# Kernel tuning notes

Measured on AMD Instinct MI355X. Metric: run time of the kernel, lower is better.

## Reference

```python
import jax, jax.numpy as jnp
import numpy as np

N, IN_DIM, MLPW, HID, NCLS = 2048, 1024, 16, 256, 4


def setup_inputs() -> dict:
    key = jax.random.key(0)
    ks = jax.random.split(key, 12)
    f32 = jnp.float32
    return {
        "x": jax.random.normal(ks[0], (N, IN_DIM), f32),
        "adj": jax.random.uniform(ks[1], (N, N), f32),
        "xdeg": jax.random.uniform(ks[2], (N, N), f32),
        "ydeg": jax.random.uniform(ks[3], (N, N), f32),
        # edge MLP([3, mlp_width, 2])
        "Wm1": jax.random.normal(ks[4], (3, MLPW), f32) * (1.0 / np.sqrt(3.0)),
        "bm1": jnp.zeros((MLPW,), f32),
        "Wm2": jax.random.normal(ks[5], (MLPW, 2), f32) * (1.0 / np.sqrt(MLPW)),
        "bm2": jnp.zeros((2,), f32),
        # GCN / dense layers (stored as [in, out]; torch Linear applies x @ W.T)
        "Wg1": jax.random.normal(ks[6], (IN_DIM, HID), f32) * (1.0 / np.sqrt(IN_DIM)),
        "Wl2": jax.random.normal(ks[7], (HID, 64), f32) * (1.0 / np.sqrt(HID)),
        "bl2": jnp.zeros((64,), f32),
        "Wg2": jax.random.normal(ks[8], (64, NCLS), f32) * (1.0 / 8.0),
    }


def reference(x, adj, xdeg, ydeg, Wm1, bm1, Wm2, bm2, Wg1, Wl2, bl2, Wg2):
    n = adj.shape[0]
    # Edge-feature MLP mask. The torch code gathers nonzero entries, runs the
    # MLP, scatters back into a zero buffer, then multiplies by adj. Computing
    # the mask densely is mathematically identical because adj * mask is zero
    # wherever adj is zero.
    feats = jnp.stack([adj, xdeg, ydeg], axis=-1)          # [N, N, 3]
    h = jax.nn.relu(feats @ Wm1 + bm1)                     # [N, N, MLPW]
    mask = jax.nn.softmax(h @ Wm2 + bm2, axis=-1)[..., 1]  # [N, N]
    A = adj * mask + jnp.eye(n, dtype=adj.dtype)
    # Symmetric-ish normalization: D_row^{-1/2} A D_col^{-1/2}
    # (the torch diag-matmul chain reduces to this row/col scaling).
    rowsum = jnp.sum(A, axis=1)
    colsum = jnp.sum(A, axis=0)
    dr = jnp.where(rowsum > 0, jax.lax.rsqrt(jnp.where(rowsum > 0, rowsum, 1.0)), 0.0)
    dc = jnp.where(colsum > 0, jax.lax.rsqrt(jnp.where(colsum > 0, colsum, 1.0)), 0.0)
    A = dr[:, None] * A * dc[None, :]
    # GCN layer 1 (dropout = identity in eval mode)
    hid = (A @ (x @ Wg1)) @ Wl2 + bl2                      # [N, 64]
    # GCN layer 2
    out = A @ (hid @ Wg2)                                  # [N, n_classes]
    return out, hid
```

## Files before the change

kernel.cpp:

```cpp
#include <hip/hip_runtime.h>

#define NN 2048
#define MLPW 16

typedef __attribute__((ext_vector_type(8))) short short8v;
typedef __attribute__((ext_vector_type(16))) float float16v;
typedef __attribute__((ext_vector_type(4))) unsigned short ushort4v;
typedef __attribute__((ext_vector_type(8))) unsigned short ushort8v;

__device__ __forceinline__ unsigned short f2b(float f) {
  unsigned int u = __float_as_uint(f);
  unsigned int r = (u + 0x7fffu + ((u >> 16) & 1u)) >> 16;
  return (unsigned short)r;
}
__device__ __forceinline__ float b2f(unsigned short u) {
  return __uint_as_float(((unsigned int)u) << 16);
}

__global__ void __launch_bounds__(256) prep_wT_kernel(
    const float* __restrict__ Wg1, unsigned short* __restrict__ wT) {
  const int n = blockIdx.x, tid = threadIdx.x;
  for (int k = tid; k < 1024; k += 256)
    wT[(size_t)n * 1024 + k] = f2b(Wg1[(size_t)k * 256 + n]);
}

__global__ void __launch_bounds__(256) edge_kernel(
    const float* __restrict__ adj, const float* __restrict__ xdeg,
    const float* __restrict__ ydeg,
    const float* __restrict__ Wm1, const float* __restrict__ bm1,
    const float* __restrict__ Wm2, const float* __restrict__ bm2,
    unsigned short* __restrict__ Abf, float* __restrict__ dr) {
  __shared__ float w1[48], b1[16], w2[32], b2s[2];
  __shared__ float wsum[4];
  const int tid = threadIdx.x;
  if (tid < 48) w1[tid] = Wm1[tid];
  if (tid < 16) b1[tid] = bm1[tid];
  if (tid < 32) w2[tid] = Wm2[tid];
  if (tid < 2) b2s[tid] = bm2[tid];
  __syncthreads();
  const int i = blockIdx.x;
  const float4* adj4 = (const float4*)(adj + (size_t)i * NN);
  const float4* xd4 = (const float4*)(xdeg + (size_t)i * NN);
  const float4* yd4 = (const float4*)(ydeg + (size_t)i * NN);
  ushort4v* A4 = (ushort4v*)(Abf + (size_t)i * NN);
  float rsum = 0.f;
  for (int j4 = tid; j4 < NN / 4; j4 += 256) {
    float4 av = adj4[j4], xv = xd4[j4], yv = yd4[j4];
    float aa[4] = {av.x, av.y, av.z, av.w};
    float xx[4] = {xv.x, xv.y, xv.z, xv.w};
    float yy[4] = {yv.x, yv.y, yv.z, yv.w};
    ushort4v oo;
#pragma unroll
    for (int e = 0; e < 4; e++) {
      float l0 = b2s[0], l1 = b2s[1];
#pragma unroll
      for (int k = 0; k < MLPW; k++) {
        float h = fmaf(aa[e], w1[k], fmaf(xx[e], w1[16 + k], fmaf(yy[e], w1[32 + k], b1[k])));
        h = fmaxf(h, 0.f);
        l0 = fmaf(h, w2[2 * k], l0);
        l1 = fmaf(h, w2[2 * k + 1], l1);
      }
      float mask = 1.f / (1.f + __expf(l0 - l1));
      float v = aa[e] * mask;
      int j = j4 * 4 + e;
      if (j == i) v += 1.f;
      oo[e] = f2b(v);
      rsum += v;
    }
    A4[j4] = oo;
  }
#pragma unroll
  for (int off = 32; off > 0; off >>= 1) rsum += __shfl_down(rsum, off);
  if ((tid & 63) == 0) wsum[tid >> 6] = rsum;
  __syncthreads();
  if (tid == 0) {
    float t = wsum[0] + wsum[1] + wsum[2] + wsum[3];
    dr[i] = t > 0.f ? rsqrtf(t) : 0.f;
  }
}

__global__ void __launch_bounds__(256) colsum_partial_kernel(
    const unsigned short* __restrict__ Abf, float* __restrict__ partial) {
  const int j = blockIdx.x * 256 + threadIdx.x;
  const int i0 = blockIdx.y * (NN / 32);
  float s = 0.f;
  for (int i = i0; i < i0 + NN / 32; i++) s += b2f(Abf[(size_t)i * NN + j]);
  partial[(size_t)blockIdx.y * NN + j] = s;
}

__global__ void __launch_bounds__(256) dc_kernel(
    const float* __restrict__ partial, float* __restrict__ dc) {
  const int j = blockIdx.x * 256 + threadIdx.x;
  float s = 0.f;
#pragma unroll
  for (int p = 0; p < 32; p++) s += partial[(size_t)p * NN + j];
  dc[j] = s > 0.f ? rsqrtf(s) : 0.f;
}

template <bool B_F32>
__global__ void __launch_bounds__(256) gemm_splitk_kernel(
    const unsigned short* __restrict__ A, const void* __restrict__ Bv,
    float* __restrict__ P, int M, int N, int K, int Kc) {
  __shared__ unsigned short As[32 * 80];
  __shared__ unsigned short Bs[128 * 80];
  const int tid = threadIdx.x;
  const int lane = tid & 63, wave = tid >> 6;
  const int l31 = lane & 31, half = lane >> 5;
  const int row0 = blockIdx.y * 32, col0 = blockIdx.x * 128;
  const int kbeg = blockIdx.z * Kc;

  float16v acc;
#pragma unroll
  for (int r = 0; r < 16; r++) acc[r] = 0.f;

  for (int k0 = 0; k0 < Kc; k0 += 64) {
    {
      const int r = tid >> 3, c = tid & 7;
      *(ushort8v*)&As[r * 80 + c * 8] =
          *(const ushort8v*)&A[(size_t)(row0 + r) * K + kbeg + k0 + c * 8];
    }
#pragma unroll
    for (int i = 0; i < 4; i++) {
      const int id = tid + i * 256;
      const int r = id >> 3, c = id & 7;
      if (B_F32) {
        const float* bp = (const float*)Bv + (size_t)(col0 + r) * K + kbeg + k0 + c * 8;
        float4 u = *(const float4*)bp, v = *(const float4*)(bp + 4);
        ushort8v pk = {f2b(u.x), f2b(u.y), f2b(u.z), f2b(u.w),
                       f2b(v.x), f2b(v.y), f2b(v.z), f2b(v.w)};
        *(ushort8v*)&Bs[r * 80 + c * 8] = pk;
      } else {
        *(ushort8v*)&Bs[r * 80 + c * 8] =
            *(const ushort8v*)&((const unsigned short*)Bv)[(size_t)(col0 + r) * K + kbeg + k0 + c * 8];
      }
    }
    __syncthreads();
#pragma unroll
    for (int ks = 0; ks < 4; ks++) {
      short8v a = *(const short8v*)&As[l31 * 80 + ks * 16 + half * 8];
      short8v b = *(const short8v*)&Bs[(wave * 32 + l31) * 80 + ks * 16 + half * 8];
      acc = __builtin_amdgcn_mfma_f32_32x32x16_bf16(a, b, acc, 0, 0, 0);
    }
    __syncthreads();
  }
  float* Pb = P + ((size_t)blockIdx.z * M + row0) * N + col0 + wave * 32 + l31;
#pragma unroll
  for (int reg = 0; reg < 16; reg++) {
    const int m = (reg & 3) + 8 * (reg >> 2) + 4 * half;
    Pb[(size_t)m * N] = acc[reg];
  }
}

__global__ void __launch_bounds__(256) reduce_xwt_kernel(
    const float* __restrict__ P, const float* __restrict__ dc,
    unsigned short* __restrict__ XWT) {
  const int t = blockIdx.x * 256 + threadIdx.x;
  const int i = t >> 8;
  const int j0 = (t & 255) * 8;
  float s[8] = {0, 0, 0, 0, 0, 0, 0, 0};
#pragma unroll
  for (int sk = 0; sk < 4; sk++) {
    const float* p = P + ((size_t)sk * 256 + i) * 2048 + j0;
    float4 u = *(const float4*)p, v = *(const float4*)(p + 4);
    s[0] += u.x; s[1] += u.y; s[2] += u.z; s[3] += u.w;
    s[4] += v.x; s[5] += v.y; s[6] += v.z; s[7] += v.w;
  }
  float4 d0 = *(const float4*)&dc[j0], d1 = *(const float4*)&dc[j0 + 4];
  ushort8v o = {f2b(s[0] * d0.x), f2b(s[1] * d0.y), f2b(s[2] * d0.z), f2b(s[3] * d0.w),
                f2b(s[4] * d1.x), f2b(s[5] * d1.y), f2b(s[6] * d1.z), f2b(s[7] * d1.w)};
  *(ushort8v*)&XWT[(size_t)i * 2048 + j0] = o;
}

__global__ void __launch_bounds__(256) tail_kernel(
    const float* __restrict__ P2, const float* __restrict__ dr,
    const float* __restrict__ dc, const float* __restrict__ Wl2,
    const float* __restrict__ bl2, const float* __restrict__ Wg2,
    float* __restrict__ hid, float* __restrict__ HW) {
  __shared__ float T1s[16][256];
  __shared__ float hidS[16][68];
  const int m0 = blockIdx.x * 16;
  const int tid = threadIdx.x;
#pragma unroll
  for (int i = 0; i < 16; i++) {
    const int idx = tid + i * 256;
    const int mi = idx >> 8, n = idx & 255;
    float s = 0.f;
#pragma unroll
    for (int sk = 0; sk < 4; sk++)
      s += P2[((size_t)sk * 2048 + m0 + mi) * 256 + n];
    T1s[mi][n] = s * dr[m0 + mi];
  }
  __syncthreads();
  const int j = tid & 63, mg = tid >> 6;
  float h[4] = {bl2[j], bl2[j], bl2[j], bl2[j]};
  for (int n = 0; n < 256; n++) {
    float w = Wl2[(size_t)n * 64 + j];
#pragma unroll
    for (int r = 0; r < 4; r++) h[r] = fmaf(T1s[mg * 4 + r][n], w, h[r]);
  }
#pragma unroll
  for (int r = 0; r < 4; r++) {
    hid[(size_t)(m0 + mg * 4 + r) * 64 + j] = h[r];
    hidS[mg * 4 + r][j] = h[r];
  }
  __syncthreads();
  if (tid < 64) {
    const int r = tid >> 2, c = tid & 3;
    float s = 0.f;
#pragma unroll
    for (int jj = 0; jj < 64; jj++) s = fmaf(hidS[r][jj], Wg2[jj * 4 + c], s);
    HW[(size_t)(m0 + r) * 4 + c] = s * dc[m0 + r];
  }
}

__global__ void __launch_bounds__(256) out_kernel(
    const unsigned short* __restrict__ Abf, const float* __restrict__ HW,
    const float* __restrict__ dr, float* __restrict__ outp) {
  const int i = blockIdx.x, tid = threadIdx.x;
  const ushort8v a8 = ((const ushort8v*)(Abf + (size_t)i * NN))[tid];
  const float4* hw4 = (const float4*)HW;
  const int j0 = tid * 8;
  float ax = 0.f, ay = 0.f, az = 0.f, aw = 0.f;
#pragma unroll
  for (int e = 0; e < 8; e++) {
    float a = b2f(a8[e]);
    float4 h = hw4[j0 + e];
    ax = fmaf(a, h.x, ax);
    ay = fmaf(a, h.y, ay);
    az = fmaf(a, h.z, az);
    aw = fmaf(a, h.w, aw);
  }
  __shared__ float red[4][256];
  red[0][tid] = ax; red[1][tid] = ay; red[2][tid] = az; red[3][tid] = aw;
  __syncthreads();
  for (int s = 128; s > 0; s >>= 1) {
    if (tid < s) {
      red[0][tid] += red[0][tid + s];
      red[1][tid] += red[1][tid + s];
      red[2][tid] += red[2][tid + s];
      red[3][tid] += red[3][tid + s];
    }
    __syncthreads();
  }
  if (tid < 4) outp[(size_t)i * 4 + tid] = dr[i] * red[tid][0];
}

extern "C" void kernel_launch(void* const* d_in, const int* in_sizes, int n_in,
                              void* d_out, int out_size, void* d_ws, size_t ws_size,
                              hipStream_t stream) {
  const float* x    = (const float*)d_in[0];
  const float* adj  = (const float*)d_in[1];
  const float* xdeg = (const float*)d_in[2];
  const float* ydeg = (const float*)d_in[3];
  const float* Wm1  = (const float*)d_in[4];
  const float* bm1  = (const float*)d_in[5];
  const float* Wm2  = (const float*)d_in[6];
  const float* bm2  = (const float*)d_in[7];
  const float* Wg1  = (const float*)d_in[8];
  const float* Wl2  = (const float*)d_in[9];
  const float* bl2  = (const float*)d_in[10];
  const float* Wg2  = (const float*)d_in[11];

  char* ws = (char*)d_ws;
  unsigned short* Abf  = (unsigned short*)(ws);
  unsigned short* Wg1T = (unsigned short*)(ws + 8388608);
  unsigned short* XWT  = (unsigned short*)(ws + 8912896);
  float* P    = (float*)(ws + 9961472);
  float* part = (float*)(ws + 18350080);
  float* dr   = (float*)(ws + 18612224);
  float* dc   = (float*)(ws + 18620416);
  float* HW   = (float*)(ws + 18628608);

  float* outp = (float*)d_out;
  float* hid  = (float*)d_out + 2048 * 4;

  prep_wT_kernel<<<256, 256, 0, stream>>>(Wg1, Wg1T);
  edge_kernel<<<NN, 256, 0, stream>>>(adj, xdeg, ydeg, Wm1, bm1, Wm2, bm2, Abf, dr);
  colsum_partial_kernel<<<dim3(NN / 256, 32), 256, 0, stream>>>(Abf, part);
  dc_kernel<<<NN / 256, 256, 0, stream>>>(part, dc);
  gemm_splitk_kernel<true><<<dim3(2048 / 128, 256 / 32, 4), 256, 0, stream>>>(
      Wg1T, x, P, 256, 2048, 1024, 256);
  reduce_xwt_kernel<<<256, 256, 0, stream>>>(P, dc, XWT);
  gemm_splitk_kernel<false><<<dim3(256 / 128, 2048 / 32, 4), 256, 0, stream>>>(
      Abf, XWT, P, 2048, 256, 2048, 512);
  tail_kernel<<<2048 / 16, 256, 0, stream>>>(P, dr, dc, Wl2, bl2, Wg2, hid, HW);
  out_kernel<<<NN, 256, 0, stream>>>(Abf, HW, dr, outp);
}
```

Before: 179.0 us.

## Tile Wg1 transpose, vectorize colsum, deepen GEMM K-tile and raise split-K

The Wg1 transpose now goes through a shared-memory tile so both reads and writes are coalesced, and the column-sum kernel reads eight bf16 values per thread with 32 row blocks. The split-K GEMM stages a 128-wide K slab per iteration, which halves the number of barriers, and the A@XW GEMM uses split-K 8 instead of 4 to launch more blocks. In exchange the GEMM uses more shared memory, which can lower occupancy, and the tail kernel has to reduce twice as many fp32 partials. The workspace layout is rearranged to hold the larger partial buffer.

```diff
diff --git a/kernel.cpp b/kernel.cpp
--- a/kernel.cpp
+++ b/kernel.cpp
@@ -19,9 +19,30 @@
 
 __global__ void __launch_bounds__(256) prep_wT_kernel(
     const float* __restrict__ Wg1, unsigned short* __restrict__ wT) {
-  const int n = blockIdx.x, tid = threadIdx.x;
-  for (int k = tid; k < 1024; k += 256)
-    wT[(size_t)n * 1024 + k] = f2b(Wg1[(size_t)k * 256 + n]);
+  __shared__ float T[64][65];
+  const int k0 = blockIdx.x * 64, n0 = blockIdx.y * 64;
+  const int tid = threadIdx.x;
+  const int kr = tid >> 2, ch = tid & 3;
+  const float* src = Wg1 + (size_t)(k0 + kr) * 256 + n0 + ch * 16;
+#pragma unroll
+  for (int q = 0; q < 4; q++) {
+    float4 v = ((const float4*)src)[q];
+    T[kr][ch * 16 + q * 4 + 0] = v.x;
+    T[kr][ch * 16 + q * 4 + 1] = v.y;
+    T[kr][ch * 16 + q * 4 + 2] = v.z;
+    T[kr][ch * 16 + q * 4 + 3] = v.w;
+  }
+  __syncthreads();
+  const int nr = kr, kc = ch;
+  ushort8v o0, o1;
+#pragma unroll
+  for (int e = 0; e < 8; e++) {
+    o0[e] = f2b(T[kc * 16 + e][nr]);
+    o1[e] = f2b(T[kc * 16 + 8 + e][nr]);
+  }
+  unsigned short* dst = wT + (size_t)(n0 + nr) * 1024 + k0 + kc * 16;
+  *(ushort8v*)dst = o0;
+  *(ushort8v*)(dst + 8) = o1;
 }
 
 __global__ void __launch_bounds__(256) edge_kernel(
@@ -79,13 +100,19 @@
   }
 }
 
-__global__ void __launch_bounds__(256) colsum_partial_kernel(
+__global__ void __launch_bounds__(256) colsum_kernel(
     const unsigned short* __restrict__ Abf, float* __restrict__ partial) {
-  const int j = blockIdx.x * 256 + threadIdx.x;
-  const int i0 = blockIdx.y * (NN / 32);
-  float s = 0.f;
-  for (int i = i0; i < i0 + NN / 32; i++) s += b2f(Abf[(size_t)i * NN + j]);
-  partial[(size_t)blockIdx.y * NN + j] = s;
+  const int j0 = threadIdx.x * 8;
+  const int i0 = blockIdx.x * 64;
+  float s[8] = {0, 0, 0, 0, 0, 0, 0, 0};
+  for (int i = 0; i < 64; i++) {
+    ushort8v a = *(const ushort8v*)&Abf[(size_t)(i0 + i) * NN + j0];
+#pragma unroll
+    for (int e = 0; e < 8; e++) s[e] += b2f(a[e]);
+  }
+  float* p = partial + (size_t)blockIdx.x * NN + j0;
+  *(float4*)p = make_float4(s[0], s[1], s[2], s[3]);
+  *(float4*)(p + 4) = make_float4(s[4], s[5], s[6], s[7]);
 }
 
 __global__ void __launch_bounds__(256) dc_kernel(
@@ -101,8 +128,9 @@
 __global__ void __launch_bounds__(256) gemm_splitk_kernel(
     const unsigned short* __restrict__ A, const void* __restrict__ Bv,
     float* __restrict__ P, int M, int N, int K, int Kc) {
-  __shared__ unsigned short As[32 * 80];
-  __shared__ unsigned short Bs[128 * 80];
+  constexpr int SW = 136;
+  __shared__ unsigned short As[32 * SW];
+  __shared__ unsigned short Bs[128 * SW];
   const int tid = threadIdx.x;
   const int lane = tid & 63, wave = tid >> 6;
   const int l31 = lane & 31, half = lane >> 5;
@@ -113,32 +141,34 @@
 #pragma unroll
   for (int r = 0; r < 16; r++) acc[r] = 0.f;
 
-  for (int k0 = 0; k0 < Kc; k0 += 64) {
-    {
-      const int r = tid >> 3, c = tid & 7;
-      *(ushort8v*)&As[r * 80 + c * 8] =
+  for (int k0 = 0; k0 < Kc; k0 += 128) {
+#pragma unroll
+    for (int i = 0; i < 2; i++) {
+      const int id = tid + i * 256;
+      const int r = id >> 4, c = id & 15;
+      *(ushort8v*)&As[r * SW + c * 8] =
           *(const ushort8v*)&A[(size_t)(row0 + r) * K + kbeg + k0 + c * 8];
     }
 #pragma unroll
-    for (int i = 0; i < 4; i++) {
+    for (int i = 0; i < 8; i++) {
       const int id = tid + i * 256;
-      const int r = id >> 3, c = id & 7;
+      const int r = id >> 4, c = id & 15;
       if (B_F32) {
         const float* bp = (const float*)Bv + (size_t)(col0 + r) * K + kbeg + k0 + c * 8;
         float4 u = *(const float4*)bp, v = *(const float4*)(bp + 4);
         ushort8v pk = {f2b(u.x), f2b(u.y), f2b(u.z), f2b(u.w),
                        f2b(v.x), f2b(v.y), f2b(v.z), f2b(v.w)};
-        *(ushort8v*)&Bs[r * 80 + c * 8] = pk;
+        *(ushort8v*)&Bs[r * SW + c * 8] = pk;
       } else {
-        *(ushort8v*)&Bs[r * 80 + c * 8] =
+        *(ushort8v*)&Bs[r * SW + c * 8] =
             *(const ushort8v*)&((const unsigned short*)Bv)[(size_t)(col0 + r) * K + kbeg + k0 + c * 8];
       }
     }
     __syncthreads();
 #pragma unroll
-    for (int ks = 0; ks < 4; ks++) {
-      short8v a = *(const short8v*)&As[l31 * 80 + ks * 16 + half * 8];
-      short8v b = *(const short8v*)&Bs[(wave * 32 + l31) * 80 + ks * 16 + half * 8];
+    for (int ks = 0; ks < 8; ks++) {
+      short8v a = *(const short8v*)&As[l31 * SW + ks * 16 + half * 8];
+      short8v b = *(const short8v*)&Bs[(wave * 32 + l31) * SW + ks * 16 + half * 8];
       acc = __builtin_amdgcn_mfma_f32_32x32x16_bf16(a, b, acc, 0, 0, 0);
     }
     __syncthreads();
@@ -186,7 +216,7 @@
     const int mi = idx >> 8, n = idx & 255;
     float s = 0.f;
 #pragma unroll
-    for (int sk = 0; sk < 4; sk++)
+    for (int sk = 0; sk < 8; sk++)
       s += P2[((size_t)sk * 2048 + m0 + mi) * 256 + n];
     T1s[mi][n] = s * dr[m0 + mi];
   }
@@ -263,26 +293,26 @@
 
   char* ws = (char*)d_ws;
   unsigned short* Abf  = (unsigned short*)(ws);
-  unsigned short* Wg1T = (unsigned short*)(ws + 8388608);
-  unsigned short* XWT  = (unsigned short*)(ws + 8912896);
-  float* P    = (float*)(ws + 9961472);
-  float* part = (float*)(ws + 18350080);
-  float* dr   = (float*)(ws + 18612224);
-  float* dc   = (float*)(ws + 18620416);
-  float* HW   = (float*)(ws + 18628608);
+  unsigned short* XWT  = (unsigned short*)(ws + 8388608);
+  float* P    = (float*)(ws + 9437184);
+  float* part = (float*)(ws + 26214400);
+  float* dr   = (float*)(ws + 26476544);
+  float* dc   = (float*)(ws + 26484736);
+  float* HW   = (float*)(ws + 26492928);
+  unsigned short* Wg1T = (unsigned short*)(ws + 26525696);
 
   float* outp = (float*)d_out;
   float* hid  = (float*)d_out + 2048 * 4;
 
-  prep_wT_kernel<<<256, 256, 0, stream>>>(Wg1, Wg1T);
+  prep_wT_kernel<<<dim3(1024 / 64, 256 / 64), 256, 0, stream>>>(Wg1, Wg1T);
   edge_kernel<<<NN, 256, 0, stream>>>(adj, xdeg, ydeg, Wm1, bm1, Wm2, bm2, Abf, dr);
-  colsum_partial_kernel<<<dim3(NN / 256, 32), 256, 0, stream>>>(Abf, part);
+  colsum_kernel<<<32, 256, 0, stream>>>(Abf, part);
   dc_kernel<<<NN / 256, 256, 0, stream>>>(part, dc);
   gemm_splitk_kernel<true><<<dim3(2048 / 128, 256 / 32, 4), 256, 0, stream>>>(
       Wg1T, x, P, 256, 2048, 1024, 256);
   reduce_xwt_kernel<<<256, 256, 0, stream>>>(P, dc, XWT);
-  gemm_splitk_kernel<false><<<dim3(256 / 128, 2048 / 32, 4), 256, 0, stream>>>(
-      Abf, XWT, P, 2048, 256, 2048, 512);
+  gemm_splitk_kernel<false><<<dim3(256 / 128, 2048 / 32, 8), 256, 0, stream>>>(
+      Abf, XWT, P, 2048, 256, 2048, 256);
   tail_kernel<<<2048 / 16, 256, 0, stream>>>(P, dr, dc, Wl2, bl2, Wg2, hid, HW);
   out_kernel<<<NN, 256, 0, stream>>>(Abf, HW, dr, outp);
 }
```

New measurement: 183.8 us. +2.7%, slower.
